# Kernel optimization log

Measured on AMD Instinct MI355X. Metric: run time of the kernel, lower is better.

Reference implementation:

```python
import jax, jax.numpy as jnp
import numpy as np

N_NODES = 100000
N_EDGES = 3200000
F_IN = 128
HID = 32
N_CLASSES = 40
NEG_SLOPE = 0.2


def _add_self_loops(edge_index, n):
    loops = jnp.arange(n, dtype=edge_index.dtype)
    src = jnp.concatenate([edge_index[0], loops])
    dst = jnp.concatenate([edge_index[1], loops])
    return src, dst


def _gat_layer(x, src, dst, W, a_src, a_dst, b, n):
    # h: [N, C]
    h = x @ W
    hs = h[src]                      # [E, C] gathered source features
    alpha_s = hs @ a_src             # [E]
    alpha_d = (h @ a_dst)[dst]       # [E]
    e = jax.nn.leaky_relu(alpha_s + alpha_d, NEG_SLOPE)
    # segment softmax over incoming edges per destination node
    m = jax.ops.segment_max(e, dst, num_segments=n)
    ex = jnp.exp(e - m[dst])
    denom = jax.ops.segment_sum(ex, dst, num_segments=n)
    alpha = ex / denom[dst]
    out = jax.ops.segment_sum(alpha[:, None] * hs, dst, num_segments=n)
    return out + b


def setup_inputs() -> dict:
    key = jax.random.key(0)
    ks = jax.random.split(key, 8)
    x = jax.random.normal(ks[0], (N_NODES, F_IN), dtype=jnp.float32)
    edge_index = jax.random.randint(ks[1], (2, N_EDGES), 0, N_NODES, dtype=jnp.int32)
    W1 = jax.random.normal(ks[2], (F_IN, HID), dtype=jnp.float32) * (1.0 / np.sqrt(F_IN))
    att_src1 = jax.random.normal(ks[3], (HID,), dtype=jnp.float32) * 0.1
    att_dst1 = jax.random.normal(ks[4], (HID,), dtype=jnp.float32) * 0.1
    b1 = jnp.zeros((HID,), dtype=jnp.float32)
    W2 = jax.random.normal(ks[5], (HID, N_CLASSES), dtype=jnp.float32) * (1.0 / np.sqrt(HID))
    att_src2 = jax.random.normal(ks[6], (N_CLASSES,), dtype=jnp.float32) * 0.1
    att_dst2 = jax.random.normal(ks[7], (N_CLASSES,), dtype=jnp.float32) * 0.1
    b2 = jnp.zeros((N_CLASSES,), dtype=jnp.float32)
    return {"x": x, "edge_index": edge_index, "W1": W1, "att_src1": att_src1,
            "att_dst1": att_dst1, "b1": b1, "W2": W2, "att_src2": att_src2,
            "att_dst2": att_dst2, "b2": b2}


def reference(x, edge_index, W1, att_src1, att_dst1, b1, W2, att_src2, att_dst2, b2):
    n = x.shape[0]
    src, dst = _add_self_loops(edge_index, n)  # PyG GATConv default add_self_loops=True
    h = _gat_layer(x, src, dst, W1, att_src1, att_dst1, b1, n)
    h = jax.nn.relu(h)  # dropout is identity in eval mode
    h = _gat_layer(h, src, dst, W2, att_src2, att_dst2, b2, n)
    h = jax.nn.relu(h)
    return jax.nn.log_softmax(h, axis=1)
```

## Files before the change

kernel.cpp:

```cpp
#include <hip/hip_runtime.h>
#include <hip/hip_bf16.h>
#include <hip/hip_fp16.h>
#include <math.h>

#define N_NODES 100000
#define N_EDGES 3200000
#define ET (N_EDGES + N_NODES)
#define F_IN 128
#define HID 32
#define NCLS 40
#define NEG 0.2f

#define NB 782
#define NBLK 782
#define CHUNK 4096
#define BCAP 5120
#define GEMM_BLKS (N_NODES / 8)

__global__ __launch_bounds__(256) void k_hist_gemm(
    const int* __restrict__ dst, int* __restrict__ Hm,
    const float* __restrict__ x, const float* __restrict__ W1,
    const float* __restrict__ a_s, const float* __restrict__ a_d,
    __half* __restrict__ h1h, float* __restrict__ s1, float* __restrict__ d1,
    const float* __restrict__ W2, const float* __restrict__ as2,
    const float* __restrict__ ad2, float* __restrict__ va_s, float* __restrict__ va_d) {
    __shared__ __align__(16) char smem[F_IN * HID * 4 + 8 * F_IN * 4];
    int t = threadIdx.x;
    if (blockIdx.x < NBLK) {
        int* hist = (int*)smem;
        int k = blockIdx.x;
        for (int i = t; i < NB; i += 256) hist[i] = 0;
        __syncthreads();
        int base = k * CHUNK;
#pragma unroll
        for (int j = 0; j < CHUNK / 256; j++) {
            int e = base + j * 256 + t;
            if (e < N_EDGES) atomicAdd(&hist[dst[e] >> 7], 1);
        }
        __syncthreads();
        for (int i = t; i < NB; i += 256) Hm[i * NBLK + k] = hist[i];
    } else if (blockIdx.x < NBLK + GEMM_BLKS) {
        float* Ws = (float*)smem;
        float* xs = Ws + F_IN * HID;
        int bb = blockIdx.x - NBLK;
        const float4* W4 = (const float4*)W1;
        float4* Ws4 = (float4*)Ws;
#pragma unroll
        for (int i = 0; i < F_IN * HID / 4 / 256; i++)
            Ws4[t + i * 256] = W4[t + i * 256];
        ((float4*)xs)[t] = ((const float4*)(x + (size_t)bb * 8 * F_IN))[t];
        __syncthreads();
        int c = t & 31, g = t >> 5;
        int v = bb * 8 + g;
        const float4* xg4 = (const float4*)(xs + g * F_IN);
        float acc = 0.f;
#pragma unroll
        for (int k4 = 0; k4 < F_IN / 4; k4++) {
            float4 xv = xg4[k4];
            int k = k4 * 4;
            acc = fmaf(xv.x, Ws[(k + 0) * HID + c], acc);
            acc = fmaf(xv.y, Ws[(k + 1) * HID + c], acc);
            acc = fmaf(xv.z, Ws[(k + 2) * HID + c], acc);
            acc = fmaf(xv.w, Ws[(k + 3) * HID + c], acc);
        }
        h1h[(size_t)v * HID + c] = __float2half(acc);
        float p = acc * a_s[c];
        float q = acc * a_d[c];
        for (int mm = 16; mm >= 1; mm >>= 1) {
            p += __shfl_xor(p, mm, 32);
            q += __shfl_xor(q, mm, 32);
        }
        if (c == 0) { s1[v] = p; d1[v] = q; }
    } else {
        if (t < HID) {
            float ps = 0.f, pd = 0.f;
            for (int c = 0; c < NCLS; c++) {
                float w = W2[t * NCLS + c];
                ps = fmaf(w, as2[c], ps);
                pd = fmaf(w, ad2[c], pd);
            }
            va_s[t] = ps;
            va_d[t] = pd;
        }
    }
}

__global__ void k_scan_a(const int* __restrict__ in, int* __restrict__ out,
                         int* __restrict__ bsums, int L) {
    __shared__ int sd[256];
    int t = threadIdx.x, b = blockIdx.x;
    int base = b * 1024 + t * 4;
    int v0 = 0, v1 = 0, v2 = 0, v3 = 0;
    if (base     < L) v0 = in[base];
    if (base + 1 < L) v1 = in[base + 1];
    if (base + 2 < L) v2 = in[base + 2];
    if (base + 3 < L) v3 = in[base + 3];
    int ts = v0 + v1 + v2 + v3;
    sd[t] = ts;
    __syncthreads();
    for (int off = 1; off < 256; off <<= 1) {
        int xx = (t >= off) ? sd[t - off] : 0;
        __syncthreads();
        sd[t] += xx;
        __syncthreads();
    }
    int ex = sd[t] - ts;
    if (t == 255) bsums[b] = sd[255];
    if (base     < L) out[base]     = ex;
    if (base + 1 < L) out[base + 1] = ex + v0;
    if (base + 2 < L) out[base + 2] = ex + v0 + v1;
    if (base + 3 < L) out[base + 3] = ex + v0 + v1 + v2;
}

__global__ void k_scan_b(const int* __restrict__ bsums, int* __restrict__ boffs, int nb) {
    __shared__ int sd[256];
    int t = threadIdx.x;
    int base = t * 4;
    int v0 = 0, v1 = 0, v2 = 0, v3 = 0;
    if (base     < nb) v0 = bsums[base];
    if (base + 1 < nb) v1 = bsums[base + 1];
    if (base + 2 < nb) v2 = bsums[base + 2];
    if (base + 3 < nb) v3 = bsums[base + 3];
    int ts = v0 + v1 + v2 + v3;
    sd[t] = ts;
    __syncthreads();
    for (int off = 1; off < 256; off <<= 1) {
        int xx = (t >= off) ? sd[t - off] : 0;
        __syncthreads();
        sd[t] += xx;
        __syncthreads();
    }
    int ex = sd[t] - ts;
    if (base     < nb) boffs[base]     = ex;
    if (base + 1 < nb) boffs[base + 1] = ex + v0;
    if (base + 2 < nb) boffs[base + 2] = ex + v0 + v1;
    if (base + 3 < nb) boffs[base + 3] = ex + v0 + v1 + v2;
}

__global__ void k_scan_c(int* __restrict__ out, const int* __restrict__ boffs, int L) {
    int i = blockIdx.x * 256 + threadIdx.x;
    if (i < L) out[i] += boffs[i >> 10];
}

__global__ __launch_bounds__(256) void kA_scatter(
    const int* __restrict__ src, const int* __restrict__ dst,
    const int* __restrict__ Sx, unsigned int* __restrict__ tmp) {
    __shared__ int hist[NB];
    __shared__ int lofs[NB];
    __shared__ int tsum[256];
    __shared__ unsigned int stage[CHUNK];
    __shared__ unsigned short bkt16[CHUNK];
    int t = threadIdx.x, k = blockIdx.x;
    for (int i = t; i < NB; i += 256) hist[i] = 0;
    __syncthreads();
    int base = k * CHUNK;
    int myd[16], mys[16];
#pragma unroll
    for (int j = 0; j < 16; j++) {
        int e = base + j * 256 + t;
        myd[j] = (e < N_EDGES) ? dst[e] : -1;
        mys[j] = (e < N_EDGES) ? src[e] : 0;
        if (myd[j] >= 0) atomicAdd(&hist[myd[j] >> 7], 1);
    }
    __syncthreads();
    int i0 = 4 * t;
    int h0 = (i0     < NB) ? hist[i0]     : 0;
    int h1 = (i0 + 1 < NB) ? hist[i0 + 1] : 0;
    int h2 = (i0 + 2 < NB) ? hist[i0 + 2] : 0;
    int h3 = (i0 + 3 < NB) ? hist[i0 + 3] : 0;
    int ts = h0 + h1 + h2 + h3;
    tsum[t] = ts;
    __syncthreads();
    for (int off = 1; off < 256; off <<= 1) {
        int xx = (t >= off) ? tsum[t - off] : 0;
        __syncthreads();
        tsum[t] += xx;
        __syncthreads();
    }
    int ex = tsum[t] - ts;
    if (i0     < NB) { lofs[i0]     = ex;                hist[i0]     = 0; }
    if (i0 + 1 < NB) { lofs[i0 + 1] = ex + h0;           hist[i0 + 1] = 0; }
    if (i0 + 2 < NB) { lofs[i0 + 2] = ex + h0 + h1;      hist[i0 + 2] = 0; }
    if (i0 + 3 < NB) { lofs[i0 + 3] = ex + h0 + h1 + h2; hist[i0 + 3] = 0; }
    __syncthreads();
#pragma unroll
    for (int j = 0; j < 16; j++) {
        if (myd[j] >= 0) {
            int bkt = myd[j] >> 7;
            int slot = lofs[bkt] + atomicAdd(&hist[bkt], 1);
            stage[slot] = ((unsigned int)(myd[j] & 127) << 17) | (unsigned int)mys[j];
            bkt16[slot] = (unsigned short)bkt;
        }
    }
    __syncthreads();
    int nvalid = min(CHUNK, N_EDGES - base);
    for (int i = t; i < nvalid; i += 256) {
        int b = bkt16[i];
        tmp[Sx[b * NBLK + k] + (i - lofs[b])] = stage[i];
    }
}

__global__ __launch_bounds__(256) void kB_sort(
    const unsigned int* __restrict__ tmp, const int* __restrict__ Sx,
    int* __restrict__ esrc, int* __restrict__ rs, int* __restrict__ deg) {
    __shared__ int ordered[BCAP + 128];
    __shared__ int cnt[128], lofs[128], cur[128], sc[128];
    int t = threadIdx.x, b = blockIdx.x;
    int myBase = Sx[b * NBLK];
    int nextBase = (b == NB - 1) ? N_EDGES : Sx[(b + 1) * NBLK];
    int cntE = nextBase - myBase;
    int nNodes = min(128, N_NODES - b * 128);
    if (t < 128) { cnt[t] = 0; cur[t] = 0; }
    __syncthreads();
    for (int i = t; i < cntE; i += 256) {
        unsigned int p = tmp[myBase + i];
        atomicAdd(&cnt[p >> 17], 1);
    }
    __syncthreads();
    int val = 0;
    if (t < 128) { val = (t < nNodes) ? cnt[t] + 1 : 0; sc[t] = val; }
    __syncthreads();
    for (int off = 1; off < 128; off <<= 1) {
        int xx = 0;
        if (t < 128 && t >= off) xx = sc[t - off];
        __syncthreads();
        if (t < 128) sc[t] += xx;
        __syncthreads();
    }
    if (t < 128) lofs[t] = sc[t] - val;
    __syncthreads();
    if (t < nNodes) ordered[lofs[t]] = b * 128 + t;
    for (int i = t; i < cntE; i += 256) {
        unsigned int p = tmp[myBase + i];
        int n = p >> 17;
        int slot = lofs[n] + 1 + atomicAdd(&cur[n], 1);
        ordered[slot] = (int)(p & 0x1FFFF);
    }
    __syncthreads();
    int gb = myBase + b * 128;
    int totOut = cntE + nNodes;
    for (int i = t; i < totOut; i += 256) esrc[gb + i] = ordered[i];
    if (t < nNodes) {
        rs[b * 128 + t] = gb + lofs[t];
        deg[b * 128 + t] = cnt[t] + 1;
    }
}

#define GATHER_BODY(SARR, TABLE)                                                  \
    float a0 = 0.f, a1 = 0.f, a2 = 0.f, a3 = 0.f,                                 \
          a4 = 0.f, a5 = 0.f, a6 = 0.f, a7 = 0.f;                                 \
    float den = 0.f;                                                              \
    int t = 0;                                                                    \
    for (; t + 16 <= cnt; t += 16) {                                              \
        int p0 = start + t + e;                                                   \
        int sa0 = esrc[p0];                                                       \
        int sa1 = esrc[p0 + 4];                                                   \
        int sa2 = esrc[p0 + 8];                                                   \
        int sa3 = esrc[p0 + 12];                                                  \
        float sv0 = SARR[sa0];                                                    \
        float sv1 = SARR[sa1];                                                    \
        float sv2 = SARR[sa2];                                                    \
        float sv3 = SARR[sa3];                                                    \
        uint4 hv0 = TABLE[(size_t)sa0 * 4 + q];                                   \
        uint4 hv1 = TABLE[(size_t)sa1 * 4 + q];                                   \
        uint4 hv2 = TABLE[(size_t)sa2 * 4 + q];                                   \
        uint4 hv3 = TABLE[(size_t)sa3 * 4 + q];                                   \
        float e0 = sv0 + dval; e0 = (e0 >= 0.f) ? e0 : NEG * e0;                  \
        float e1 = sv1 + dval; e1 = (e1 >= 0.f) ? e1 : NEG * e1;                  \
        float e2 = sv2 + dval; e2 = (e2 >= 0.f) ? e2 : NEG * e2;                  \
        float e3 = sv3 + dval; e3 = (e3 >= 0.f) ? e3 : NEG * e3;                  \
        float w0 = __expf(e0);                                                    \
        float w1 = __expf(e1);                                                    \
        float w2 = __expf(e2);                                                    \
        float w3 = __expf(e3);                                                    \
        den += (w0 + w1) + (w2 + w3);                                             \
        ACC8(w0, hv0); ACC8(w1, hv1); ACC8(w2, hv2); ACC8(w3, hv3);               \
    }                                                                             \
    for (; t < cnt; t += 4) {                                                     \
        int idx = t + e;                                                          \
        int sa = 0;                                                               \
        float w = 0.f;                                                            \
        if (idx < cnt) {                                                          \
            sa = esrc[start + idx];                                               \
            float ev = SARR[sa] + dval;                                           \
            ev = (ev >= 0.f) ? ev : NEG * ev;                                     \
            w = __expf(ev);                                                       \
        }                                                                         \
        uint4 hv = TABLE[(size_t)sa * 4 + q];                                     \
        ACC8(w, hv);                                                              \
        den += w;                                                                 \
    }

#define ACC8(W, HV)                                                               \
    {                                                                             \
        float2 f0 = __half22float2(*(const __half2*)&(HV).x);                     \
        float2 f1 = __half22float2(*(const __half2*)&(HV).y);                     \
        float2 f2 = __half22float2(*(const __half2*)&(HV).z);                     \
        float2 f3 = __half22float2(*(const __half2*)&(HV).w);                     \
        a0 = fmaf((W), f0.x, a0); a1 = fmaf((W), f0.y, a1);                       \
        a2 = fmaf((W), f1.x, a2); a3 = fmaf((W), f1.y, a3);                       \
        a4 = fmaf((W), f2.x, a4); a5 = fmaf((W), f2.y, a5);                       \
        a6 = fmaf((W), f3.x, a6); a7 = fmaf((W), f3.y, a7);                       \
    }

__global__ __launch_bounds__(256) void k_fused1(
    const int* __restrict__ rs, const int* __restrict__ deg, const int* __restrict__ esrc,
    const uint4* __restrict__ h1r, const float* __restrict__ s1, const float* __restrict__ d1,
    const float* __restrict__ b1, const float* __restrict__ va_s, const float* __restrict__ va_d,
    uint4* __restrict__ hrr, float* __restrict__ s2, float* __restrict__ d2) {
    int tid = threadIdx.x;
    int sub = tid & 15;
    int q = sub & 3;
    int e = sub >> 2;
    int v = blockIdx.x * 16 + (tid >> 4);
    int start = rs[v];
    int cnt = deg[v];
    float dval = d1[v];
    GATHER_BODY(s1, h1r)
#pragma unroll
    for (int off = 4; off <= 8; off <<= 1) {
        a0 += __shfl_xor(a0, off); a1 += __shfl_xor(a1, off);
        a2 += __shfl_xor(a2, off); a3 += __shfl_xor(a3, off);
        a4 += __shfl_xor(a4, off); a5 += __shfl_xor(a5, off);
        a6 += __shfl_xor(a6, off); a7 += __shfl_xor(a7, off);
        den += __shfl_xor(den, off);
    }
    if (e == 0) {
        float iden = 1.f / den;
        const float4* b4 = (const float4*)(b1 + q * 8);
        float4 bA = b4[0], bB = b4[1];
        float o0 = fmaxf(a0 * iden + bA.x, 0.f);
        float o1 = fmaxf(a1 * iden + bA.y, 0.f);
        float o2 = fmaxf(a2 * iden + bA.z, 0.f);
        float o3 = fmaxf(a3 * iden + bA.w, 0.f);
        float o4 = fmaxf(a4 * iden + bB.x, 0.f);
        float o5 = fmaxf(a5 * iden + bB.y, 0.f);
        float o6 = fmaxf(a6 * iden + bB.z, 0.f);
        float o7 = fmaxf(a7 * iden + bB.w, 0.f);
        __half2 p0 = __floats2half2_rn(o0, o1);
        __half2 p1 = __floats2half2_rn(o2, o3);
        __half2 p2 = __floats2half2_rn(o4, o5);
        __half2 p3 = __floats2half2_rn(o6, o7);
        uint4 ov;
        ov.x = *(const unsigned int*)&p0;
        ov.y = *(const unsigned int*)&p1;
        ov.z = *(const unsigned int*)&p2;
        ov.w = *(const unsigned int*)&p3;
        hrr[(size_t)v * 4 + q] = ov;
        const float4* vs4 = (const float4*)(va_s + q * 8);
        const float4* vd4 = (const float4*)(va_d + q * 8);
        float4 sA = vs4[0], sB = vs4[1], dA = vd4[0], dB = vd4[1];
        float ps = o0 * sA.x + o1 * sA.y + o2 * sA.z + o3 * sA.w
                 + o4 * sB.x + o5 * sB.y + o6 * sB.z + o7 * sB.w;
        float pd = o0 * dA.x + o1 * dA.y + o2 * dA.z + o3 * dA.w
                 + o4 * dB.x + o5 * dB.y + o6 * dB.z + o7 * dB.w;
        ps += __shfl_xor(ps, 1); pd += __shfl_xor(pd, 1);
        ps += __shfl_xor(ps, 2); pd += __shfl_xor(pd, 2);
        if (q == 0) { s2[v] = ps; d2[v] = pd; }
    }
}

__global__ __launch_bounds__(256) void k_fused2(
    const int* __restrict__ rs, const int* __restrict__ deg, const int* __restrict__ esrc,
    const uint4* __restrict__ hrr, const float* __restrict__ s2, const float* __restrict__ d2,
    const float* __restrict__ W2, const float* __restrict__ b2, float* __restrict__ out) {
    __shared__ float W2s[HID * NCLS];
    __shared__ float hragg[16][HID];
    __shared__ float zbuf[16][NCLS];
    __shared__ float gm[16], gl[16];
    int tid = threadIdx.x;
    for (int i = tid; i < HID * NCLS; i += 256) W2s[i] = W2[i];
    int sub = tid & 15;
    int q = sub & 3;
    int e = sub >> 2;
    int node = tid >> 4;
    int v = blockIdx.x * 16 + node;
    int start = rs[v];
    int cnt = deg[v];
    float dval = d2[v];
    GATHER_BODY(s2, hrr)
#pragma unroll
    for (int off = 4; off <= 8; off <<= 1) {
        a0 += __shfl_xor(a0, off); a1 += __shfl_xor(a1, off);
        a2 += __shfl_xor(a2, off); a3 += __shfl_xor(a3, off);
        a4 += __shfl_xor(a4, off); a5 += __shfl_xor(a5, off);
        a6 += __shfl_xor(a6, off); a7 += __shfl_xor(a7, off);
        den += __shfl_xor(den, off);
    }
    if (e == 0) {
        float iden = 1.f / den;
        int cb = q * 8;
        hragg[node][cb + 0] = a0 * iden;
        hragg[node][cb + 1] = a1 * iden;
        hragg[node][cb + 2] = a2 * iden;
        hragg[node][cb + 3] = a3 * iden;
        hragg[node][cb + 4] = a4 * iden;
        hragg[node][cb + 5] = a5 * iden;
        hragg[node][cb + 6] = a6 * iden;
        hragg[node][cb + 7] = a7 * iden;
    }
    __syncthreads();
    for (int oi = tid; oi < 16 * NCLS; oi += 256) {
        int n = oi / NCLS, c = oi % NCLS;
        float z = 0.f;
#pragma unroll
        for (int k = 0; k < HID; k++)
            z = fmaf(hragg[n][k], W2s[k * NCLS + c], z);
        zbuf[n][c] = fmaxf(z + b2[c], 0.f);
    }
    __syncthreads();
    if (tid < 16) {
        float mx = -INFINITY;
        for (int c = 0; c < NCLS; c++) mx = fmaxf(mx, zbuf[tid][c]);
        float se = 0.f;
        for (int c = 0; c < NCLS; c++) se += __expf(zbuf[tid][c] - mx);
        gm[tid] = mx;
        gl[tid] = logf(se);
    }
    __syncthreads();
    for (int oi = tid; oi < 16 * NCLS; oi += 256) {
        int n = oi / NCLS, c = oi % NCLS;
        out[(size_t)(blockIdx.x * 16 + n) * NCLS + c] = zbuf[n][c] - gm[n] - gl[n];
    }
}


extern "C" void kernel_launch(void* const* d_in, const int* in_sizes, int n_in,
                              void* d_out, int out_size, void* d_ws, size_t ws_size,
                              hipStream_t stream) {
    (void)in_sizes; (void)n_in; (void)out_size; (void)ws_size;
    const float* x   = (const float*)d_in[0];
    const int*   ei  = (const int*)d_in[1];
    const float* W1  = (const float*)d_in[2];
    const float* as1 = (const float*)d_in[3];
    const float* ad1 = (const float*)d_in[4];
    const float* b1  = (const float*)d_in[5];
    const float* W2  = (const float*)d_in[6];
    const float* as2 = (const float*)d_in[7];
    const float* ad2 = (const float*)d_in[8];
    const float* b2  = (const float*)d_in[9];
    float* out = (float*)d_out;
    const int* srcA = ei;
    const int* dstA = ei + N_EDGES;

    char* w = (char*)d_ws;
    size_t off = 0;
    auto alloc = [&](size_t bytes) {
        char* p = w + off;
        off = (off + bytes + 255) & ~(size_t)255;
        return p;
    };
    int* esrc     = (int*)alloc((size_t)ET * 4);
    int* rs       = (int*)alloc((size_t)N_NODES * 4);
    int* deg      = (int*)alloc((size_t)N_NODES * 4);
    char* region1 = alloc((size_t)N_NODES * HID * 4);
    float* s1     = (float*)alloc((size_t)N_NODES * 4);
    float* d1     = (float*)alloc((size_t)N_NODES * 4);
    char* region2 = alloc((size_t)N_EDGES * 4 + 1024);
    float* s2     = (float*)alloc((size_t)N_NODES * 4);
    float* d2     = (float*)alloc((size_t)N_NODES * 4);
    float* va_s   = (float*)alloc(HID * 4);
    float* va_d   = (float*)alloc(HID * 4);
    int* bsums    = (int*)alloc(1024 * 4);
    int* boffs    = (int*)alloc(1024 * 4);

    const int L = NB * NBLK;
    int* Hm = (int*)region1;
    int* Sx = Hm + ((L + 63) & ~63);
    __half* h1h = (__half*)(region1 + (size_t)N_NODES * HID * 2);
    unsigned int* tmp = (unsigned int*)region2;
    __half* hrt = (__half*)region2;

    int nb1 = (L + 1023) / 1024;
    hipLaunchKernelGGL(k_hist_gemm, dim3(NBLK + GEMM_BLKS + 1), dim3(256), 0, stream,
                       dstA, Hm, x, W1, as1, ad1, h1h, s1, d1,
                       W2, as2, ad2, va_s, va_d);
    hipLaunchKernelGGL(k_scan_a, dim3(nb1), dim3(256), 0, stream, Hm, Sx, bsums, L);
    hipLaunchKernelGGL(k_scan_b, dim3(1), dim3(256), 0, stream, bsums, boffs, nb1);
    hipLaunchKernelGGL(k_scan_c, dim3((L + 255) / 256), dim3(256), 0, stream, Sx, boffs, L);
    hipLaunchKernelGGL(kA_scatter, dim3(NBLK), dim3(256), 0, stream, srcA, dstA, Sx, tmp);
    hipLaunchKernelGGL(kB_sort, dim3(NB), dim3(256), 0, stream, tmp, Sx, esrc, rs, deg);
    hipLaunchKernelGGL(k_fused1, dim3(N_NODES / 16), dim3(256), 0, stream, rs, deg, esrc,
                       (const uint4*)h1h, s1, d1, b1, va_s, va_d,
                       (uint4*)hrt, s2, d2);
    hipLaunchKernelGGL(k_fused2, dim3(N_NODES / 16), dim3(256), 0, stream, rs, deg, esrc,
                       (const uint4*)hrt, s2, d2, W2, b2, out);
}
```

Baseline: 300.2 us.

## Fold scan fixup into consumers, halve edge chunk size, vectorize edge loads

Drops the k_scan_c pass by having the scatter and sort kernels add the block offset (boffs) themselves when reading the partially scanned Sx. Halves CHUNK so twice as many scatter and histogram blocks run, each holding fewer registers, and widens the scan to 8 elements per thread so the block-sum count stays small. Loads src/dst as int4 and precomputes a per-bucket global base in shared memory so the final scatter does one indirection. This doubles the size of the histogram matrix that must be scanned, and Hm is moved into region2.

Result: slower. 311.6 us (+3.8%).

```diff
diff --git a/kernel.cpp b/kernel.cpp
--- a/kernel.cpp
+++ b/kernel.cpp
@@ -12,8 +12,8 @@
 #define NEG 0.2f
 
 #define NB 782
-#define NBLK 782
-#define CHUNK 4096
+#define CHUNK 2048
+#define NBLK ((N_EDGES + CHUNK - 1) / CHUNK)
 #define BCAP 5120
 #define GEMM_BLKS (N_NODES / 8)
 
@@ -31,11 +31,17 @@
         int k = blockIdx.x;
         for (int i = t; i < NB; i += 256) hist[i] = 0;
         __syncthreads();
-        int base = k * CHUNK;
-#pragma unroll
-        for (int j = 0; j < CHUNK / 256; j++) {
-            int e = base + j * 256 + t;
-            if (e < N_EDGES) atomicAdd(&hist[dst[e] >> 7], 1);
+        int b4 = k * (CHUNK / 4);
+#pragma unroll
+        for (int j = 0; j < CHUNK / 4 / 256; j++) {
+            int i4 = b4 + j * 256 + t;
+            if (i4 < N_EDGES / 4) {
+                int4 d = ((const int4*)dst)[i4];
+                atomicAdd(&hist[d.x >> 7], 1);
+                atomicAdd(&hist[d.y >> 7], 1);
+                atomicAdd(&hist[d.z >> 7], 1);
+                atomicAdd(&hist[d.w >> 7], 1);
+            }
         }
         __syncthreads();
         for (int i = t; i < NB; i += 256) Hm[i * NBLK + k] = hist[i];
@@ -89,13 +95,14 @@
                          int* __restrict__ bsums, int L) {
     __shared__ int sd[256];
     int t = threadIdx.x, b = blockIdx.x;
-    int base = b * 1024 + t * 4;
-    int v0 = 0, v1 = 0, v2 = 0, v3 = 0;
-    if (base     < L) v0 = in[base];
-    if (base + 1 < L) v1 = in[base + 1];
-    if (base + 2 < L) v2 = in[base + 2];
-    if (base + 3 < L) v3 = in[base + 3];
-    int ts = v0 + v1 + v2 + v3;
+    int base = b * 2048 + t * 8;
+    int v[8];
+    int ts = 0;
+#pragma unroll
+    for (int u = 0; u < 8; u++) {
+        v[u] = (base + u < L) ? in[base + u] : 0;
+        ts += v[u];
+    }
     sd[t] = ts;
     __syncthreads();
     for (int off = 1; off < 256; off <<= 1) {
@@ -104,12 +111,13 @@
         sd[t] += xx;
         __syncthreads();
     }
-    int ex = sd[t] - ts;
+    int run = sd[t] - ts;
     if (t == 255) bsums[b] = sd[255];
-    if (base     < L) out[base]     = ex;
-    if (base + 1 < L) out[base + 1] = ex + v0;
-    if (base + 2 < L) out[base + 2] = ex + v0 + v1;
-    if (base + 3 < L) out[base + 3] = ex + v0 + v1 + v2;
+#pragma unroll
+    for (int u = 0; u < 8; u++) {
+        if (base + u < L) out[base + u] = run;
+        run += v[u];
+    }
 }
 
 __global__ void k_scan_b(const int* __restrict__ bsums, int* __restrict__ boffs, int nb) {
@@ -137,14 +145,10 @@
     if (base + 3 < nb) boffs[base + 3] = ex + v0 + v1 + v2;
 }
 
-__global__ void k_scan_c(int* __restrict__ out, const int* __restrict__ boffs, int L) {
-    int i = blockIdx.x * 256 + threadIdx.x;
-    if (i < L) out[i] += boffs[i >> 10];
-}
-
 __global__ __launch_bounds__(256) void kA_scatter(
     const int* __restrict__ src, const int* __restrict__ dst,
-    const int* __restrict__ Sx, unsigned int* __restrict__ tmp) {
+    const int* __restrict__ Sx, const int* __restrict__ boffs,
+    unsigned int* __restrict__ tmp) {
     __shared__ int hist[NB];
     __shared__ int lofs[NB];
     __shared__ int tsum[256];
@@ -153,14 +157,26 @@
     int t = threadIdx.x, k = blockIdx.x;
     for (int i = t; i < NB; i += 256) hist[i] = 0;
     __syncthreads();
-    int base = k * CHUNK;
-    int myd[16], mys[16];
-#pragma unroll
-    for (int j = 0; j < 16; j++) {
-        int e = base + j * 256 + t;
-        myd[j] = (e < N_EDGES) ? dst[e] : -1;
-        mys[j] = (e < N_EDGES) ? src[e] : 0;
-        if (myd[j] >= 0) atomicAdd(&hist[myd[j] >> 7], 1);
+    int myd[8], mys[8];
+    int b4 = k * (CHUNK / 4);
+#pragma unroll
+    for (int j = 0; j < CHUNK / 4 / 256; j++) {
+        int i4 = b4 + j * 256 + t;
+        if (i4 < N_EDGES / 4) {
+            int4 d = ((const int4*)dst)[i4];
+            int4 s = ((const int4*)src)[i4];
+            myd[j * 4 + 0] = d.x; mys[j * 4 + 0] = s.x;
+            myd[j * 4 + 1] = d.y; mys[j * 4 + 1] = s.y;
+            myd[j * 4 + 2] = d.z; mys[j * 4 + 2] = s.z;
+            myd[j * 4 + 3] = d.w; mys[j * 4 + 3] = s.w;
+            atomicAdd(&hist[d.x >> 7], 1);
+            atomicAdd(&hist[d.y >> 7], 1);
+            atomicAdd(&hist[d.z >> 7], 1);
+            atomicAdd(&hist[d.w >> 7], 1);
+        } else {
+#pragma unroll
+            for (int u = 0; u < 4; u++) { myd[j * 4 + u] = -1; mys[j * 4 + u] = 0; }
+        }
     }
     __syncthreads();
     int i0 = 4 * t;
@@ -184,7 +200,7 @@
     if (i0 + 3 < NB) { lofs[i0 + 3] = ex + h0 + h1 + h2; hist[i0 + 3] = 0; }
     __syncthreads();
 #pragma unroll
-    for (int j = 0; j < 16; j++) {
+    for (int j = 0; j < 8; j++) {
         if (myd[j] >= 0) {
             int bkt = myd[j] >> 7;
             int slot = lofs[bkt] + atomicAdd(&hist[bkt], 1);
@@ -193,21 +209,31 @@
         }
     }
     __syncthreads();
-    int nvalid = min(CHUNK, N_EDGES - base);
-    for (int i = t; i < nvalid; i += 256) {
-        int b = bkt16[i];
-        tmp[Sx[b * NBLK + k] + (i - lofs[b])] = stage[i];
-    }
+    for (int b = t; b < NB; b += 256) {
+        int idx = b * NBLK + k;
+        hist[b] = Sx[idx] + boffs[idx >> 11] - lofs[b];
+    }
+    __syncthreads();
+    int nvalid = min(CHUNK, N_EDGES - k * CHUNK);
+    for (int i = t; i < nvalid; i += 256)
+        tmp[hist[bkt16[i]] + i] = stage[i];
 }
 
 __global__ __launch_bounds__(256) void kB_sort(
     const unsigned int* __restrict__ tmp, const int* __restrict__ Sx,
+    const int* __restrict__ boffs,
     int* __restrict__ esrc, int* __restrict__ rs, int* __restrict__ deg) {
     __shared__ int ordered[BCAP + 128];
     __shared__ int cnt[128], lofs[128], cur[128], sc[128];
     int t = threadIdx.x, b = blockIdx.x;
-    int myBase = Sx[b * NBLK];
-    int nextBase = (b == NB - 1) ? N_EDGES : Sx[(b + 1) * NBLK];
+    int idx0 = b * NBLK;
+    int myBase = Sx[idx0] + boffs[idx0 >> 11];
+    int nextBase;
+    if (b == NB - 1) nextBase = N_EDGES;
+    else {
+        int idx1 = (b + 1) * NBLK;
+        nextBase = Sx[idx1] + boffs[idx1 >> 11];
+    }
     int cntE = nextBase - myBase;
     int nNodes = min(128, N_NODES - b * 128);
     if (t < 128) { cnt[t] = 0; cur[t] = 0; }
@@ -465,21 +491,20 @@
     int* boffs    = (int*)alloc(1024 * 4);
 
     const int L = NB * NBLK;
-    int* Hm = (int*)region1;
-    int* Sx = Hm + ((L + 63) & ~63);
+    int* Hm = (int*)region2;
+    int* Sx = (int*)region1;
     __half* h1h = (__half*)(region1 + (size_t)N_NODES * HID * 2);
     unsigned int* tmp = (unsigned int*)region2;
     __half* hrt = (__half*)region2;
 
-    int nb1 = (L + 1023) / 1024;
+    int nb1 = (L + 2047) / 2048;
     hipLaunchKernelGGL(k_hist_gemm, dim3(NBLK + GEMM_BLKS + 1), dim3(256), 0, stream,
                        dstA, Hm, x, W1, as1, ad1, h1h, s1, d1,
                        W2, as2, ad2, va_s, va_d);
     hipLaunchKernelGGL(k_scan_a, dim3(nb1), dim3(256), 0, stream, Hm, Sx, bsums, L);
     hipLaunchKernelGGL(k_scan_b, dim3(1), dim3(256), 0, stream, bsums, boffs, nb1);
-    hipLaunchKernelGGL(k_scan_c, dim3((L + 255) / 256), dim3(256), 0, stream, Sx, boffs, L);
-    hipLaunchKernelGGL(kA_scatter, dim3(NBLK), dim3(256), 0, stream, srcA, dstA, Sx, tmp);
-    hipLaunchKernelGGL(kB_sort, dim3(NB), dim3(256), 0, stream, tmp, Sx, esrc, rs, deg);
+    hipLaunchKernelGGL(kA_scatter, dim3(NBLK), dim3(256), 0, stream, srcA, dstA, Sx, boffs, tmp);
+    hipLaunchKernelGGL(kB_sort, dim3(NB), dim3(256), 0, stream, tmp, Sx, boffs, esrc, rs, deg);
     hipLaunchKernelGGL(k_fused1, dim3(N_NODES / 16), dim3(256), 0, stream, rs, deg, esrc,
                        (const uint4*)h1h, s1, d1, b1, va_s, va_d,
                        (uint4*)hrt, s2, d2);
```
